# Kernel optimization log

Measured on AMD Instinct MI355X. Metric: run time of the kernel, lower is better.

The kernel has to match this reference:

```python
import jax, jax.numpy as jnp
import numpy as np

DIM = 256
NUM_HEADS = 4
HEAD_DIM = DIM // NUM_HEADS
EPS = 1e-5


def setup_inputs() -> dict:
    key = jax.random.key(0)
    ks = jax.random.split(key, 8)
    B, N, C = 8, 2048, DIM
    s = 0.02
    return {
        "x": jax.random.normal(ks[0], (B, N, C), jnp.float32),
        "qkv_w": jax.random.normal(ks[1], (C, 3 * C), jnp.float32) * s,
        "qkv_b": jnp.zeros((3 * C,), jnp.float32),
        "proj_w": jax.random.normal(ks[2], (C, C), jnp.float32) * s,
        "proj_b": jnp.zeros((C,), jnp.float32),
        "ln1_g": jnp.ones((C,), jnp.float32),
        "ln1_b": jnp.zeros((C,), jnp.float32),
        "ln2_g": jnp.ones((C,), jnp.float32),
        "ln2_b": jnp.zeros((C,), jnp.float32),
        "mlp_w1": jax.random.normal(ks[3], (C, 2 * C), jnp.float32) * s,
        "mlp_b1": jnp.zeros((2 * C,), jnp.float32),
        "mlp_w2": jax.random.normal(ks[4], (2 * C, C), jnp.float32) * s,
        "mlp_b2": jnp.zeros((C,), jnp.float32),
    }


def _layernorm(x, g, b):
    mu = jnp.mean(x, axis=-1, keepdims=True)
    var = jnp.mean(jnp.square(x - mu), axis=-1, keepdims=True)
    return (x - mu) * jax.lax.rsqrt(var + EPS) * g + b


def reference(x, qkv_w, qkv_b, proj_w, proj_b, ln1_g, ln1_b, ln2_g, ln2_b,
              mlp_w1, mlp_b1, mlp_w2, mlp_b2):
    B, N, C = x.shape
    H, D = NUM_HEADS, HEAD_DIM
    shortcut = x
    h = _layernorm(x, ln1_g, ln1_b)
    qkv = (h @ qkv_w + qkv_b).reshape(B, N, 3, H, D)
    q = qkv[:, :, 0].transpose(0, 2, 1, 3)  # [B,H,N,D]
    k = qkv[:, :, 1].transpose(0, 2, 1, 3)
    v = qkv[:, :, 2].transpose(0, 2, 1, 3)
    attn = jnp.einsum('bhnd,bhmd->bhnm', q, k) * (D ** -0.5)
    attn = jax.nn.softmax(attn, axis=-1)  # dropout = identity (eval mode)
    o = jnp.einsum('bhnm,bhmd->bhnd', attn, v)
    o = o.transpose(0, 2, 1, 3).reshape(B, N, C)
    x = o @ proj_w + proj_b + shortcut
    h2 = _layernorm(x, ln2_g, ln2_b)
    mlp = jax.nn.gelu(h2 @ mlp_w1 + mlp_b1, approximate=False) @ mlp_w2 + mlp_b2
    return x + mlp
```

## Files before the change

kernel.cpp:

```cpp
#include <hip/hip_runtime.h>

typedef __bf16 bf16;
typedef __bf16 bf16x8 __attribute__((ext_vector_type(8)));
typedef __bf16 bf16x4 __attribute__((ext_vector_type(4)));
typedef float  f32x4  __attribute__((ext_vector_type(4)));
typedef unsigned u32x2 __attribute__((ext_vector_type(2)));

typedef __attribute__((address_space(1))) const void GASV;
typedef __attribute__((address_space(3))) void LASV;

__device__ __forceinline__ void gload16(const void* g, void* l) {
  __builtin_amdgcn_global_load_lds((GASV*)g, (LASV*)l, 16, 0, 0);
}

constexpr float CEXP = 0.125f * 1.44269504088896340736f;

__global__ __launch_bounds__(256) void wconv_all(const float* __restrict__ qkv_w,
                                                 const float* __restrict__ proj_w,
                                                 const float* __restrict__ w1,
                                                 const float* __restrict__ w2,
                                                 bf16* __restrict__ Wtqkv,
                                                 bf16* __restrict__ WtP,
                                                 bf16* __restrict__ Wt1,
                                                 bf16* __restrict__ Wt2) {
  const int idx = blockIdx.x * 256 + threadIdx.x;
  if (idx < 196608) {
    const int k = idx & 255, n = idx >> 8;
    Wtqkv[idx] = (bf16)qkv_w[k * 768 + n];
  } else if (idx < 262144) {
    const int i = idx - 196608, k = i & 255, n = i >> 8;
    WtP[i] = (bf16)proj_w[k * 256 + n];
  } else if (idx < 393216) {
    const int i = idx - 262144, k = i & 255, n = i >> 8;
    Wt1[i] = (bf16)w1[k * 512 + n];
  } else {
    const int i = idx - 393216, k = i & 511, n = i >> 9;
    Wt2[i] = (bf16)w2[k * 256 + n];
  }
}

__global__ __launch_bounds__(256) void ln_fwd(const float* __restrict__ x,
                                              const float* __restrict__ gam,
                                              const float* __restrict__ bet,
                                              bf16* __restrict__ out) {
  const int lane = threadIdx.x & 63;
  const int w = threadIdx.x >> 6;
  const size_t row = (size_t)blockIdx.x * 4 + w;
  const float4 v = *(const float4*)(x + row * 256 + lane * 4);
  float s1 = v.x + v.y + v.z + v.w;
  float s2 = v.x * v.x + v.y * v.y + v.z * v.z + v.w * v.w;
#pragma unroll
  for (int m = 1; m < 64; m <<= 1) {
    s1 += __shfl_xor(s1, m);
    s2 += __shfl_xor(s2, m);
  }
  const float mu = s1 * (1.0f / 256.0f);
  const float var = s2 * (1.0f / 256.0f) - mu * mu;
  const float rs = rsqrtf(var + 1e-5f);
  const float4 g4 = *(const float4*)(gam + lane * 4);
  const float4 b4 = *(const float4*)(bet + lane * 4);
  bf16x4 o;
  o[0] = (bf16)((v.x - mu) * rs * g4.x + b4.x);
  o[1] = (bf16)((v.y - mu) * rs * g4.y + b4.y);
  o[2] = (bf16)((v.z - mu) * rs * g4.z + b4.z);
  o[3] = (bf16)((v.w - mu) * rs * g4.w + b4.w);
  *(bf16x4*)(out + row * 256 + lane * 4) = o;
}

template <int EPI>
__global__ __launch_bounds__(256) void gemm_bt(const bf16* __restrict__ A,
                                               const bf16* __restrict__ Bt,
                                               const float* __restrict__ bias,
                                               const float* __restrict__ res,
                                               void* __restrict__ outp,
                                               int M, int N, int K) {
  __shared__ bf16 Al[2][8192];
  __shared__ bf16 Bl[2][8192];
  const int tid = threadIdx.x;
  const int lane = tid & 63;
  const int wid = tid >> 6;
  const int wm = wid >> 1, wn = wid & 1;
  const int nbm = M >> 7;
  const int bm = (int)blockIdx.x % nbm;
  const int bn = (int)blockIdx.x / nbm;
  const int m0 = bm << 7, n0 = bn << 7;
  const int nk = K >> 6;

  f32x4 acc[4][4];
#pragma unroll
  for (int i = 0; i < 4; ++i)
#pragma unroll
    for (int j = 0; j < 4; ++j) acc[i][j] = (f32x4){0.f, 0.f, 0.f, 0.f};

  auto stage = [&](int t, int s) {
    const int k0 = t << 6;
#pragma unroll
    for (int p = 0; p < 4; ++p) {
      const int idx = p * 4096 + tid * 16;
      const int row = idx >> 7;
      const int colb = idx & 127;
      gload16((const char*)(A + ((size_t)(m0 + row) * K + k0)) + colb,
              (char*)&Al[s][0] + p * 4096 + ((tid >> 6) << 10));
      gload16((const char*)(Bt + ((size_t)(n0 + row) * K + k0)) + colb,
              (char*)&Bl[s][0] + p * 4096 + ((tid >> 6) << 10));
    }
  };

  stage(0, 0);
  asm volatile("s_waitcnt vmcnt(0)" ::: "memory");
  __syncthreads();

  for (int t = 0; t < nk; ++t) {
    if (t + 1 < nk) stage(t + 1, (t + 1) & 1);
    const bf16* pa = &Al[t & 1][0] + (wm * 64 + (lane & 15)) * 64 + ((lane >> 4) << 3);
    const bf16* pb = &Bl[t & 1][0] + (wn * 64 + (lane & 15)) * 64 + ((lane >> 4) << 3);
    bf16x8 av[4][2], bv[4][2];
#pragma unroll
    for (int f = 0; f < 4; ++f)
#pragma unroll
      for (int ks = 0; ks < 2; ++ks) {
        av[f][ks] = *(const bf16x8*)(pa + f * 1024 + ks * 32);
        bv[f][ks] = *(const bf16x8*)(pb + f * 1024 + ks * 32);
      }
    __builtin_amdgcn_s_setprio(1);
#pragma unroll
    for (int fm = 0; fm < 4; ++fm)
#pragma unroll
      for (int fn = 0; fn < 4; ++fn) {
        acc[fm][fn] = __builtin_amdgcn_mfma_f32_16x16x32_bf16(av[fm][0], bv[fn][0], acc[fm][fn], 0, 0, 0);
        acc[fm][fn] = __builtin_amdgcn_mfma_f32_16x16x32_bf16(av[fm][1], bv[fn][1], acc[fm][fn], 0, 0, 0);
      }
    __builtin_amdgcn_s_setprio(0);
    asm volatile("s_waitcnt vmcnt(0)" ::: "memory");
    __syncthreads();
  }

#pragma unroll
  for (int fm = 0; fm < 4; ++fm)
#pragma unroll
    for (int fn = 0; fn < 4; ++fn) {
      const int r0 = m0 + wm * 64 + fm * 16 + ((lane >> 4) << 2);
      const int c = n0 + wn * 64 + fn * 16 + (lane & 15);
#pragma unroll
      for (int j = 0; j < 4; ++j) {
        const int r = r0 + j;
        const float v = acc[fm][fn][j];
        if constexpr (EPI == 0) {
          ((bf16*)outp)[(size_t)r * N + c] = (bf16)(v + bias[c]);
        } else if constexpr (EPI == 1) {
          ((bf16*)outp)[(size_t)r * 2048 + ((size_t)(c >> 11)) * 524288 + (c & 2047)] =
              (bf16)(v + bias[r]);
        } else if constexpr (EPI == 2) {
          ((float*)outp)[(size_t)r * N + c] = v + bias[c] + res[(size_t)r * N + c];
        } else {
          const float u = v + bias[c];
          ((bf16*)outp)[(size_t)r * N + c] = (bf16)(u * 0.5f * (1.0f + erff(u * 0.70710678118f)));
        }
      }
    }
}

__global__ __launch_bounds__(256) void attn_fwd(const bf16* __restrict__ qk,
                                                const bf16* __restrict__ vT,
                                                bf16* __restrict__ po,
                                                float* __restrict__ pstats) {
  __shared__ bf16 Kl[2][4096];
  __shared__ bf16 Vl[2][4096];
  __shared__ bf16 Pl[4][1024];
  const int tid = threadIdx.x;
  const int lane = tid & 63;
  const int w = tid >> 6;
  const int g = lane >> 4;
  const int qi = lane & 15;
  const int bid = (int)blockIdx.x;
  const int bh = bid & 31;
  const int qt = (bid >> 5) & 15;
  const int s = bid >> 9;
  const int b = bh >> 2, h = bh & 3;

  const size_t qrow0 = (size_t)b * 2048 + qt * 128 + w * 32 + qi;
  bf16x8 qf[2][2];
#pragma unroll
  for (int f = 0; f < 2; ++f) {
    const bf16* qp = qk + (qrow0 + f * 16) * 512 + h * 64 + g * 8;
    qf[f][0] = *(const bf16x8*)qp;
    qf[f][1] = *(const bf16x8*)(qp + 32);
  }

  float mrun[2] = {0.f, 0.f};
  float lsum[2] = {0.f, 0.f};
  f32x4 o[4][2];
#pragma unroll
  for (int i = 0; i < 4; ++i)
#pragma unroll
    for (int f = 0; f < 2; ++f) o[i][f] = (f32x4){0.f, 0.f, 0.f, 0.f};

  constexpr float THR = 8.0f / CEXP;

  const char* kbase = (const char*)qk + ((size_t)b * 2048) * 1024 + 512 + h * 128 +
                      (size_t)s * 16 * 65536;
  const char* vbase = (const char*)vT + (size_t)bh * 262144 + (size_t)s * 16 * 128;
  const char* ks[2];
  const char* vs[2];
#pragma unroll
  for (int i = 0; i < 2; ++i) {
    const int fk = i * 2 + (w >> 1);
    const int half = w & 1;
    ks[i] = kbase + (fk * 16 + qi) * 1024 + half * 64 + g * 16;
    vs[i] = vbase + (size_t)(fk * 16 + qi) * 4096 + half * 64 + g * 16;
  }
  char* const pw = (char*)&Pl[w][0];
  int paddrb[2];
#pragma unroll
  for (int bb = 0; bb < 2; ++bb)
    paddrb[bb] = (bb * 2 + (g >> 1)) * 256 + qi * 16 + (g & 1) * 8;
  const char* const prd = pw + lane * 16;

  auto stage = [&](int slot) {
    char* kd = (char*)&Kl[0][0] + slot * 8192 + w * 1024;
    char* vd = (char*)&Vl[0][0] + slot * 8192 + w * 1024;
    gload16(ks[0], kd);
    gload16(ks[1], kd + 4096);
    gload16(vs[0], vd);
    gload16(vs[1], vd + 4096);
    ks[0] += 65536; ks[1] += 65536;
    vs[0] += 128;   vs[1] += 128;
  };

  stage(0);
  asm volatile("s_waitcnt vmcnt(0)" ::: "memory");
  __builtin_amdgcn_s_barrier();

  for (int t = 0; t < 16; ++t) {
    if (t < 15) stage((t + 1) & 1);
    const char* kb = (const char*)&Kl[0][0] + (t & 1) * 8192 + lane * 16;
    f32x4 st[4][2];
    __builtin_amdgcn_s_setprio(1);
#pragma unroll
    for (int fk = 0; fk < 4; ++fk) {
      const bf16x8 k0 = *(const bf16x8*)(kb + fk * 2048);
      const bf16x8 k1 = *(const bf16x8*)(kb + fk * 2048 + 1024);
#pragma unroll
      for (int f = 0; f < 2; ++f) {
        f32x4 z = (f32x4){0.f, 0.f, 0.f, 0.f};
        st[fk][f] = __builtin_amdgcn_mfma_f32_16x16x32_bf16(k0, qf[f][0], z, 0, 0, 0);
        st[fk][f] = __builtin_amdgcn_mfma_f32_16x16x32_bf16(k1, qf[f][1], st[fk][f], 0, 0, 0);
      }
    }
    __builtin_amdgcn_s_setprio(0);
    float pmax[2];
#pragma unroll
    for (int f = 0; f < 2; ++f) {
      float m0 = fmaxf(fmaxf(st[0][f][0], st[0][f][1]), fmaxf(st[0][f][2], st[0][f][3]));
      float m1 = fmaxf(fmaxf(st[1][f][0], st[1][f][1]), fmaxf(st[1][f][2], st[1][f][3]));
      float m2 = fmaxf(fmaxf(st[2][f][0], st[2][f][1]), fmaxf(st[2][f][2], st[2][f][3]));
      float m3 = fmaxf(fmaxf(st[3][f][0], st[3][f][1]), fmaxf(st[3][f][2], st[3][f][3]));
      pmax[f] = fmaxf(fmaxf(m0, m1), fmaxf(m2, m3));
    }
    if (!__all(pmax[0] <= mrun[0] + THR && pmax[1] <= mrun[1] + THR)) {
#pragma unroll
      for (int f = 0; f < 2; ++f) {
        float mt = fmaxf(pmax[f], __shfl_xor(pmax[f], 16));
        mt = fmaxf(mt, __shfl_xor(mt, 32));
        const float mnew = fmaxf(mrun[f], mt);
        const float alpha = exp2f(CEXP * (mrun[f] - mnew));
        lsum[f] *= alpha;
#pragma unroll
        for (int fd = 0; fd < 4; ++fd)
#pragma unroll
          for (int j = 0; j < 4; ++j) o[fd][f][j] *= alpha;
        mrun[f] = mnew;
      }
    }
    unsigned pk[4][2][2];
#pragma unroll
    for (int f = 0; f < 2; ++f) {
      const float negcm = -CEXP * mrun[f];
      float ts = 0.f;
#pragma unroll
      for (int fk = 0; fk < 4; ++fk)
#pragma unroll
        for (int jp = 0; jp < 2; ++jp) {
          const float p0 = exp2f(fmaf(st[fk][f][2 * jp], CEXP, negcm));
          const float p1 = exp2f(fmaf(st[fk][f][2 * jp + 1], CEXP, negcm));
          ts += p0 + p1;
          union { bf16 h2[2]; unsigned u; } cv;
          cv.h2[0] = (bf16)p0;
          cv.h2[1] = (bf16)p1;
          pk[fk][f][jp] = cv.u;
        }
      lsum[f] += ts;
    }
    const char* vb = (const char*)&Vl[0][0] + (t & 1) * 8192 + lane * 16;
#pragma unroll
    for (int ksl = 0; ksl < 2; ++ksl) {
#pragma unroll
      for (int bb = 0; bb < 2; ++bb) {
        const int fk = 2 * ksl + bb;
#pragma unroll
        for (int f = 0; f < 2; ++f) {
          u32x2 pv2;
          pv2[0] = pk[fk][f][0];
          pv2[1] = pk[fk][f][1];
          *(u32x2*)(pw + f * 1024 + paddrb[bb]) = pv2;
        }
      }
      bf16x8 pa[2];
#pragma unroll
      for (int f = 0; f < 2; ++f) pa[f] = *(const bf16x8*)(prd + f * 1024);
      __builtin_amdgcn_s_setprio(1);
#pragma unroll
      for (int fd = 0; fd < 4; ++fd) {
        const bf16x8 vv = *(const bf16x8*)(vb + fd * 2048 + ksl * 1024);
#pragma unroll
        for (int f = 0; f < 2; ++f)
          o[fd][f] = __builtin_amdgcn_mfma_f32_16x16x32_bf16(vv, pa[f], o[fd][f], 0, 0, 0);
      }
      __builtin_amdgcn_s_setprio(0);
    }
    asm volatile("s_waitcnt vmcnt(0)" ::: "memory");
    __builtin_amdgcn_s_barrier();
  }

#pragma unroll
  for (int f = 0; f < 2; ++f) {
    float l = lsum[f];
    l += __shfl_xor(l, 16);
    l += __shfl_xor(l, 32);
    lsum[f] = l;
  }
  if (g == 0) {
#pragma unroll
    for (int f = 0; f < 2; ++f) {
      float2 sv;
      sv.x = mrun[f];
      sv.y = lsum[f];
      *(float2*)(pstats + (((size_t)s * 32 + bh) * 2048 + qt * 128 + w * 32 + f * 16 + qi) * 2) = sv;
    }
  }
#pragma unroll
  for (int f = 0; f < 2; ++f) {
    bf16* const orow = po + ((size_t)s * 16384 + qrow0 + f * 16) * 256 + h * 64 + g * 4;
#pragma unroll
    for (int fd = 0; fd < 4; ++fd) {
      bf16x4 ov;
#pragma unroll
      for (int j = 0; j < 4; ++j) ov[j] = (bf16)o[fd][f][j];
      *(bf16x4*)(orow + fd * 16) = ov;
    }
  }
}

__global__ __launch_bounds__(256) void attn_merge(const bf16* __restrict__ po,
                                                  const float* __restrict__ pstats,
                                                  bf16* __restrict__ ob) {
  const int idx = blockIdx.x * 256 + threadIdx.x;
  const int r = idx >> 6;
  const int cq = (idx & 63) * 4;
  const int h = cq >> 6;
  const int bh = (r >> 11) * 4 + h;
  const int ql = r & 2047;
  const float2 s0 = *(const float2*)(pstats + (((size_t)bh) * 2048 + ql) * 2);
  const float2 s1 = *(const float2*)(pstats + (((size_t)32 + bh) * 2048 + ql) * 2);
  const float M = fmaxf(s0.x, s1.x);
  const float a0 = exp2f(CEXP * (s0.x - M));
  const float a1 = exp2f(CEXP * (s1.x - M));
  const float inv = 1.0f / (s0.y * a0 + s1.y * a1);
  const bf16x4 p0 = *(const bf16x4*)(po + (size_t)r * 256 + cq);
  const bf16x4 p1 = *(const bf16x4*)(po + ((size_t)16384 + r) * 256 + cq);
  bf16x4 ov;
#pragma unroll
  for (int j = 0; j < 4; ++j)
    ov[j] = (bf16)(((float)p0[j] * a0 + (float)p1[j] * a1) * inv);
  *(bf16x4*)(ob + (size_t)r * 256 + cq) = ov;
}

extern "C" void kernel_launch(void* const* d_in, const int* in_sizes, int n_in,
                              void* d_out, int out_size, void* d_ws, size_t ws_size,
                              hipStream_t stream) {
  const float* x      = (const float*)d_in[0];
  const float* qkv_w  = (const float*)d_in[1];
  const float* qkv_b  = (const float*)d_in[2];
  const float* proj_w = (const float*)d_in[3];
  const float* proj_b = (const float*)d_in[4];
  const float* ln1_g  = (const float*)d_in[5];
  const float* ln1_b  = (const float*)d_in[6];
  const float* ln2_g  = (const float*)d_in[7];
  const float* ln2_b  = (const float*)d_in[8];
  const float* mlp_w1 = (const float*)d_in[9];
  const float* mlp_b1 = (const float*)d_in[10];
  const float* mlp_w2 = (const float*)d_in[11];
  const float* mlp_b2 = (const float*)d_in[12];
  float* out = (float*)d_out;

  char* ws = (char*)d_ws;
  bf16* Wtqkv = (bf16*)(ws);
  bf16* WtP   = (bf16*)(ws + 393216);
  bf16* Wt1   = (bf16*)(ws + 524288);
  bf16* Wt2   = (bf16*)(ws + 786432);
  bf16* h     = (bf16*)(ws + 1048576);
  bf16* qkb   = (bf16*)(ws + 9437184);
  bf16* vT    = (bf16*)(ws + 26214400);
  bf16* obuf  = (bf16*)(ws + 34603008);
  float* x2   = (float*)(ws + 42991616);
  bf16* po    = (bf16*)(ws + 42991616);
  float* pstats = (float*)(ws + 59768832);
  bf16* a1 = qkb;
  bf16* h2 = h;

  wconv_all<<<2048, 256, 0, stream>>>(qkv_w, proj_w, mlp_w1, mlp_w2, Wtqkv, WtP, Wt1, Wt2);

  ln_fwd<<<4096, 256, 0, stream>>>(x, ln1_g, ln1_b, h);
  gemm_bt<0><<<512, 256, 0, stream>>>(h, Wtqkv, qkv_b, nullptr, qkb, 16384, 512, 256);
  gemm_bt<1><<<256, 256, 0, stream>>>(Wtqkv + 512 * 256, h, qkv_b + 512, nullptr, vT, 256, 16384, 256);
  attn_fwd<<<1024, 256, 0, stream>>>(qkb, vT, po, pstats);
  attn_merge<<<4096, 256, 0, stream>>>(po, pstats, obuf);
  gemm_bt<2><<<256, 256, 0, stream>>>(obuf, WtP, proj_b, x, x2, 16384, 256, 256);
  ln_fwd<<<4096, 256, 0, stream>>>(x2, ln2_g, ln2_b, h2);
  gemm_bt<3><<<512, 256, 0, stream>>>(h2, Wt1, mlp_b1, nullptr, a1, 16384, 512, 256);
  gemm_bt<2><<<256, 256, 0, stream>>>(a1, Wt2, mlp_b2, x2, out, 16384, 256, 512);
}
```

Baseline: 175.4 us.

## Shrink GEMM tiles to 64x64 with fragment-order LDS layout and tiled weight transpose

Replaces the 128x128-tile GEMM with a 64x64-tile variant so the skinny GEMMs launch four times as many blocks, which improves occupancy and CU coverage on the many-CU device. Global-to-LDS loads are rearranged so each wave writes MFMA-fragment-ordered chunks, making LDS reads contiguous per lane, with source pointers precomputed and advanced per K step. The weight conversion kernel now transposes through a padded shared-memory tile to coalesce reads and writes. The trade-off is less data reuse per tile (more global/L2 traffic) and barriers that are no longer __syncthreads.

```diff
diff --git a/kernel.cpp b/kernel.cpp
--- a/kernel.cpp
+++ b/kernel.cpp
@@ -23,19 +23,28 @@
                                                  bf16* __restrict__ WtP,
                                                  bf16* __restrict__ Wt1,
                                                  bf16* __restrict__ Wt2) {
-  const int idx = blockIdx.x * 256 + threadIdx.x;
-  if (idx < 196608) {
-    const int k = idx & 255, n = idx >> 8;
-    Wtqkv[idx] = (bf16)qkv_w[k * 768 + n];
-  } else if (idx < 262144) {
-    const int i = idx - 196608, k = i & 255, n = i >> 8;
-    WtP[i] = (bf16)proj_w[k * 256 + n];
-  } else if (idx < 393216) {
-    const int i = idx - 262144, k = i & 255, n = i >> 8;
-    Wt1[i] = (bf16)w1[k * 512 + n];
-  } else {
-    const int i = idx - 393216, k = i & 511, n = i >> 9;
-    Wt2[i] = (bf16)w2[k * 256 + n];
+  __shared__ float td[32][33];
+  const int t = blockIdx.x;
+  const float* src;
+  bf16* dst;
+  int Kin, Nin, kt, nt;
+  if (t < 192)      { src = qkv_w; dst = Wtqkv; Kin = 256; Nin = 768; kt = t & 7;          nt = t >> 3; }
+  else if (t < 256) { src = proj_w; dst = WtP;  Kin = 256; Nin = 256; kt = (t - 192) & 7;  nt = (t - 192) >> 3; }
+  else if (t < 384) { src = w1;    dst = Wt1;   Kin = 256; Nin = 512; kt = (t - 256) & 7;  nt = (t - 256) >> 3; }
+  else              { src = w2;    dst = Wt2;   Kin = 512; Nin = 256; kt = (t - 384) & 15; nt = (t - 384) >> 4; }
+  const int tid = threadIdx.x;
+  {
+    const int r = tid >> 3, c4 = (tid & 7) << 2;
+    const float4 v = *(const float4*)(src + (size_t)(kt * 32 + r) * Nin + nt * 32 + c4);
+    td[r][c4 + 0] = v.x; td[r][c4 + 1] = v.y; td[r][c4 + 2] = v.z; td[r][c4 + 3] = v.w;
+  }
+  __syncthreads();
+  {
+    const int n = tid >> 3, k4 = (tid & 7) << 2;
+    bf16x4 o;
+#pragma unroll
+    for (int i = 0; i < 4; ++i) o[i] = (bf16)td[k4 + i][n];
+    *(bf16x4*)(dst + (size_t)(nt * 32 + n) * Kin + kt * 32 + k4) = o;
   }
 }
 
@@ -68,79 +77,86 @@
 }
 
 template <int EPI>
-__global__ __launch_bounds__(256) void gemm_bt(const bf16* __restrict__ A,
-                                               const bf16* __restrict__ Bt,
-                                               const float* __restrict__ bias,
-                                               const float* __restrict__ res,
-                                               void* __restrict__ outp,
-                                               int M, int N, int K) {
-  __shared__ bf16 Al[2][8192];
-  __shared__ bf16 Bl[2][8192];
+__global__ __launch_bounds__(256) void gemm64(const bf16* __restrict__ A,
+                                              const bf16* __restrict__ Bt,
+                                              const float* __restrict__ bias,
+                                              const float* __restrict__ res,
+                                              void* __restrict__ outp,
+                                              int M, int N, int K) {
+  __shared__ bf16 Al[2][4096];
+  __shared__ bf16 Bl[2][4096];
   const int tid = threadIdx.x;
   const int lane = tid & 63;
-  const int wid = tid >> 6;
-  const int wm = wid >> 1, wn = wid & 1;
-  const int nbm = M >> 7;
+  const int W = tid >> 6;
+  const int wm = W >> 1, wn = W & 1;
+  const int nbm = M >> 6;
   const int bm = (int)blockIdx.x % nbm;
   const int bn = (int)blockIdx.x / nbm;
-  const int m0 = bm << 7, n0 = bn << 7;
+  const int m0 = bm << 6, n0 = bn << 6;
   const int nk = K >> 6;
 
-  f32x4 acc[4][4];
-#pragma unroll
-  for (int i = 0; i < 4; ++i)
-#pragma unroll
-    for (int j = 0; j < 4; ++j) acc[i][j] = (f32x4){0.f, 0.f, 0.f, 0.f};
-
-  auto stage = [&](int t, int s) {
-    const int k0 = t << 6;
-#pragma unroll
-    for (int p = 0; p < 4; ++p) {
-      const int idx = p * 4096 + tid * 16;
-      const int row = idx >> 7;
-      const int colb = idx & 127;
-      gload16((const char*)(A + ((size_t)(m0 + row) * K + k0)) + colb,
-              (char*)&Al[s][0] + p * 4096 + ((tid >> 6) << 10));
-      gload16((const char*)(Bt + ((size_t)(n0 + row) * K + k0)) + colb,
-              (char*)&Bl[s][0] + p * 4096 + ((tid >> 6) << 10));
-    }
+  const char* asrc[2];
+  const char* bsrc[2];
+#pragma unroll
+  for (int p = 0; p < 2; ++p) {
+    const int s = W + 4 * p;
+    const int row = (s >> 2) * 32 + (((s >> 1) & 1) << 4) + (lane & 15);
+    const int kb = (((s & 1) << 5) + ((lane >> 4) << 3)) * 2;
+    asrc[p] = (const char*)(A + (size_t)(m0 + row) * K) + kb;
+    bsrc[p] = (const char*)(Bt + (size_t)(n0 + row) * K) + kb;
+  }
+
+  auto stage = [&](int sl) {
+    char* ad = (char*)&Al[sl][0] + W * 1024;
+    char* bd = (char*)&Bl[sl][0] + W * 1024;
+    gload16(asrc[0], ad);
+    gload16(asrc[1], ad + 4096);
+    gload16(bsrc[0], bd);
+    gload16(bsrc[1], bd + 4096);
+    asrc[0] += 128; asrc[1] += 128; bsrc[0] += 128; bsrc[1] += 128;
   };
 
-  stage(0, 0);
+  f32x4 acc[2][2];
+#pragma unroll
+  for (int i = 0; i < 2; ++i)
+#pragma unroll
+    for (int j = 0; j < 2; ++j) acc[i][j] = (f32x4){0.f, 0.f, 0.f, 0.f};
+
+  stage(0);
   asm volatile("s_waitcnt vmcnt(0)" ::: "memory");
-  __syncthreads();
+  __builtin_amdgcn_s_barrier();
 
   for (int t = 0; t < nk; ++t) {
-    if (t + 1 < nk) stage(t + 1, (t + 1) & 1);
-    const bf16* pa = &Al[t & 1][0] + (wm * 64 + (lane & 15)) * 64 + ((lane >> 4) << 3);
-    const bf16* pb = &Bl[t & 1][0] + (wn * 64 + (lane & 15)) * 64 + ((lane >> 4) << 3);
-    bf16x8 av[4][2], bv[4][2];
-#pragma unroll
-    for (int f = 0; f < 4; ++f)
+    if (t + 1 < nk) stage((t + 1) & 1);
+    const char* pa = (const char*)&Al[t & 1][0] + wm * 4096 + lane * 16;
+    const char* pb = (const char*)&Bl[t & 1][0] + wn * 4096 + lane * 16;
+    bf16x8 av[2][2], bv[2][2];
+#pragma unroll
+    for (int f = 0; f < 2; ++f)
 #pragma unroll
       for (int ks = 0; ks < 2; ++ks) {
-        av[f][ks] = *(const bf16x8*)(pa + f * 1024 + ks * 32);
-        bv[f][ks] = *(const bf16x8*)(pb + f * 1024 + ks * 32);
+        av[f][ks] = *(const bf16x8*)(pa + (f * 2 + ks) * 1024);
+        bv[f][ks] = *(const bf16x8*)(pb + (f * 2 + ks) * 1024);
       }
     __builtin_amdgcn_s_setprio(1);
 #pragma unroll
-    for (int fm = 0; fm < 4; ++fm)
-#pragma unroll
-      for (int fn = 0; fn < 4; ++fn) {
+    for (int fm = 0; fm < 2; ++fm)
+#pragma unroll
+      for (int fn = 0; fn < 2; ++fn) {
         acc[fm][fn] = __builtin_amdgcn_mfma_f32_16x16x32_bf16(av[fm][0], bv[fn][0], acc[fm][fn], 0, 0, 0);
         acc[fm][fn] = __builtin_amdgcn_mfma_f32_16x16x32_bf16(av[fm][1], bv[fn][1], acc[fm][fn], 0, 0, 0);
       }
     __builtin_amdgcn_s_setprio(0);
     asm volatile("s_waitcnt vmcnt(0)" ::: "memory");
-    __syncthreads();
-  }
-
-#pragma unroll
-  for (int fm = 0; fm < 4; ++fm)
-#pragma unroll
-    for (int fn = 0; fn < 4; ++fn) {
-      const int r0 = m0 + wm * 64 + fm * 16 + ((lane >> 4) << 2);
-      const int c = n0 + wn * 64 + fn * 16 + (lane & 15);
+    __builtin_amdgcn_s_barrier();
+  }
+
+#pragma unroll
+  for (int fm = 0; fm < 2; ++fm)
+#pragma unroll
+    for (int fn = 0; fn < 2; ++fn) {
+      const int r0 = m0 + wm * 32 + fm * 16 + ((lane >> 4) << 2);
+      const int c = n0 + wn * 32 + fn * 16 + (lane & 15);
 #pragma unroll
       for (int j = 0; j < 4; ++j) {
         const int r = r0 + j;
@@ -408,15 +424,15 @@
   bf16* a1 = qkb;
   bf16* h2 = h;
 
-  wconv_all<<<2048, 256, 0, stream>>>(qkv_w, proj_w, mlp_w1, mlp_w2, Wtqkv, WtP, Wt1, Wt2);
+  wconv_all<<<512, 256, 0, stream>>>(qkv_w, proj_w, mlp_w1, mlp_w2, Wtqkv, WtP, Wt1, Wt2);
 
   ln_fwd<<<4096, 256, 0, stream>>>(x, ln1_g, ln1_b, h);
-  gemm_bt<0><<<512, 256, 0, stream>>>(h, Wtqkv, qkv_b, nullptr, qkb, 16384, 512, 256);
-  gemm_bt<1><<<256, 256, 0, stream>>>(Wtqkv + 512 * 256, h, qkv_b + 512, nullptr, vT, 256, 16384, 256);
+  gemm64<0><<<2048, 256, 0, stream>>>(h, Wtqkv, qkv_b, nullptr, qkb, 16384, 512, 256);
+  gemm64<1><<<1024, 256, 0, stream>>>(Wtqkv + 512 * 256, h, qkv_b + 512, nullptr, vT, 256, 16384, 256);
   attn_fwd<<<1024, 256, 0, stream>>>(qkb, vT, po, pstats);
   attn_merge<<<4096, 256, 0, stream>>>(po, pstats, obuf);
-  gemm_bt<2><<<256, 256, 0, stream>>>(obuf, WtP, proj_b, x, x2, 16384, 256, 256);
+  gemm64<2><<<1024, 256, 0, stream>>>(obuf, WtP, proj_b, x, x2, 16384, 256, 256);
   ln_fwd<<<4096, 256, 0, stream>>>(x2, ln2_g, ln2_b, h2);
-  gemm_bt<3><<<512, 256, 0, stream>>>(h2, Wt1, mlp_b1, nullptr, a1, 16384, 512, 256);
-  gemm_bt<2><<<256, 256, 0, stream>>>(a1, Wt2, mlp_b2, x2, out, 16384, 256, 512);
-}
+  gemm64<3><<<2048, 256, 0, stream>>>(h2, Wt1, mlp_b1, nullptr, a1, 16384, 512, 256);
+  gemm64<2><<<1024, 256, 0, stream>>>(a1, Wt2, mlp_b2, x2, out, 16384, 256, 512);
+}
```

Measured after the change: 194.0 us. 1.11x slower.
